# Optimization experiments

Hardware: AMD Instinct MI355X
Metric: run time of the kernel (lower is better)

The kernel has to match this reference:

```python
import jax, jax.numpy as jnp
import numpy as np

N = 50000      # nodes
E = 500000     # edges
IN = 256       # input feature dim
HID = 64       # hidden (per-head) dim, layer 1
H1 = 4         # heads, layer 1
NC = 64        # num_classes (layer 2 out, 1 head)
ED = 32        # edge_dim
T = 8          # num_etypes
SLOPE = 0.2    # leakyrelu negative slope


def setup_inputs() -> dict:
    key = jax.random.key(0)
    ks = jax.random.split(key, 20)
    p = lambda k, shape: (jax.random.normal(k, shape, jnp.float32) * 0.05)
    return {
        "h": jax.random.normal(ks[0], (N, IN), jnp.float32),
        "row": jax.random.randint(ks[1], (E,), 0, N, jnp.int32),   # src
        "col": jax.random.randint(ks[2], (E,), 0, N, jnp.int32),   # dst
        "etype": jax.random.randint(ks[3], (E,), 0, T, jnp.int32),
        # layer 1 (4 heads, no residual, elu activation)
        "edge_emb1": p(ks[4], (T, ED)),
        "W1": p(ks[5], (IN, HID * H1)),
        "Wr1": p(ks[6], (T, ED, ED * H1)),      # TypedLinear per-etype weight
        "a_l1": p(ks[7], (H1, HID)),
        "a_r1": p(ks[8], (H1, HID)),
        "a_e1": p(ks[9], (H1, ED)),
        # layer 2 (1 head, residual Linear, no activation)
        "edge_emb2": p(ks[10], (T, ED)),
        "W2": p(ks[11], (HID * H1, NC)),
        "Wr2": p(ks[12], (T, ED, ED)),
        "a_l2": p(ks[13], (1, NC)),
        "a_r2": p(ks[14], (1, NC)),
        "a_e2": p(ks[15], (1, ED)),
        "res_W2": p(ks[16], (HID * H1, NC)),
        "res_b2": p(ks[17], (NC,)),
    }


def _simple_hgn_conv(h, row, col, etype, edge_emb, W, Wr, a_l, a_r, a_e,
                     res_W, res_b, apply_act):
    """One SimpleHGNConv layer. h:[N,in], returns [N, out_dim*H] (D-major, H-minor
    layout, matching emb.permute(0,2,1).view in the torch code)."""
    H, D = a_l.shape            # num_heads, out_dim
    n = h.shape[0]
    emb = (h @ W).reshape(n, H, D)                     # [N,H,D]
    emb = jnp.where(jnp.isnan(emb), 0.0, emb)
    # TypedLinear: edge_emb[etype] @ Wr[etype]; only T distinct rows -> per-type GEMM
    ee = jnp.einsum('te,teo->to', edge_emb, Wr).reshape(T, H, ED)  # [T,H,ED]
    h_l = jnp.einsum('nhd,hd->nh', emb, a_l)[row]      # [E,H]
    h_r = jnp.einsum('nhd,hd->nh', emb, a_r)[col]      # [E,H]
    h_e = jnp.einsum('thd,hd->th', ee, a_e)[etype]     # [E,H]
    att = jax.nn.leaky_relu(h_l + h_r + h_e, SLOPE)    # [E,H]
    # edge_softmax: normalize over incoming edges of each destination node (col)
    seg_max = jax.ops.segment_max(att, col, num_segments=n)   # [N,H]
    att = jnp.exp(att - seg_max[col])
    seg_sum = jax.ops.segment_sum(att, col, num_segments=n)   # [N,H]
    alpha = att / seg_sum[col]                          # [E,H]
    # u_mul_e + sum aggregation
    msg = emb[row] * alpha[:, :, None]                  # [E,H,D]
    out = jax.ops.segment_sum(msg, col, num_segments=n) # [N,H,D]
    out = out.transpose(0, 2, 1).reshape(n, D * H)      # D-major layout
    if res_W is not None:
        out = out + h @ res_W + res_b
    if apply_act:
        out = jax.nn.elu(out)
    return out


def reference(h, row, col, etype,
              edge_emb1, W1, Wr1, a_l1, a_r1, a_e1,
              edge_emb2, W2, Wr2, a_l2, a_r2, a_e2, res_W2, res_b2):
    h1 = _simple_hgn_conv(h, row, col, etype, edge_emb1, W1, Wr1,
                          a_l1, a_r1, a_e1, None, None, True)
    h2 = _simple_hgn_conv(h1, row, col, etype, edge_emb2, W2, Wr2,
                          a_l2, a_r2, a_e2, res_W2, res_b2, False)
    # split by node type (first half type 'l', second half type 'v')
    return (h2[: N // 2], h2[N // 2 :])
```

## Files before the change

### kernel.cpp

```cpp
#include <hip/hip_runtime.h>
#include <hip/hip_bf16.h>

typedef __bf16 bf16x8 __attribute__((ext_vector_type(8)));
typedef float f32x4 __attribute__((ext_vector_type(4)));

#define IN_DIM 256
#define NT 8

__device__ __forceinline__ float b2f(unsigned short u) {
  union { unsigned int i; float f; } x; x.i = ((unsigned int)u) << 16; return x.f;
}
__device__ __forceinline__ float lo2f(unsigned int w) {
  union { unsigned int i; float f; } x; x.i = w << 16; return x.f;
}
__device__ __forceinline__ float hi2f(unsigned int w) {
  union { unsigned int i; float f; } x; x.i = w & 0xFFFF0000u; return x.f;
}
__device__ __forceinline__ unsigned short f2b(float f) {
  union { float f; unsigned int i; } u; u.f = f;
  unsigned int r = u.i + 0x7FFF + ((u.i >> 16) & 1);
  return (unsigned short)(r >> 16);
}
__device__ __forceinline__ float lrelu(float x) { return x >= 0.f ? x : 0.2f * x; }
__device__ __forceinline__ float ldf(const void* p, size_t i, int isf32) {
  return isf32 ? ((const float*)p)[i] : b2f(((const unsigned short*)p)[i]);
}

__global__ void detect_kernel(const unsigned int* __restrict__ hw, int* __restrict__ flag) {
  int tid = threadIdx.x;
  int bad = 0;
  for (int i = 0; i < 4; i++) {
    unsigned int w = hw[tid * 4 + i];
    unsigned int e = (w & 0x7FFFu) >> 7;
    if (e >= 0xC0u) bad++;
  }
#pragma unroll
  for (int off = 32; off; off >>= 1) bad += __shfl_xor(bad, off);
  if (tid == 0) *flag = (bad > 8) ? 1 : 0;
}

__global__ void prep_all_kernel(const void* __restrict__ W1, const void* __restrict__ W2,
                                const void* __restrict__ rW2,
                                const void* __restrict__ al1, const void* __restrict__ ar1,
                                const void* __restrict__ al2, const void* __restrict__ ar2,
                                const void* __restrict__ ee1, const void* __restrict__ Wr1,
                                const void* __restrict__ ae1,
                                const void* __restrict__ ee2, const void* __restrict__ Wr2,
                                const void* __restrict__ ae2,
                                unsigned short* __restrict__ W1t,
                                unsigned short* __restrict__ W2t,
                                float* __restrict__ a2l, float* __restrict__ a2r,
                                float* __restrict__ he1, float* __restrict__ he2,
                                float* __restrict__ alD, float* __restrict__ arD,
                                const int* __restrict__ dflag) {
  int isf32 = *dflag;
  int b = blockIdx.x, tid = threadIdx.x;
  if (b < 384) {
    int j = b, k = tid;
    if (j < 256) {
      int src = (j & 3) * 64 + (j >> 2);
      W1t[j * 256 + k] = f2b(ldf(W1, (size_t)k * 256 + src, isf32));
    } else {
      int o = j - 256;
      float v = (o < 64) ? ldf(W2, (size_t)k * 64 + o, isf32)
                         : ldf(rW2, (size_t)k * 64 + (o - 64), isf32);
      W2t[o * 256 + k] = f2b(v);
    }
  } else if (b < 448) {
    int k = (b - 384) * 4 + (tid >> 6), d = tid & 63;
    float w2 = ldf(W2, (size_t)k * 64 + d, isf32);
    float l2 = w2 * ldf(al2, d, isf32);
    float r2 = w2 * ldf(ar2, d, isf32);
#pragma unroll
    for (int off = 32; off; off >>= 1) { l2 += __shfl_xor(l2, off); r2 += __shfl_xor(r2, off); }
    if (d == 0) { a2l[k] = l2; a2r[k] = r2; }
  } else {
    int bid = b - 448;
    int t = tid >> 5, d = tid & 31;
    if (bid < 4) {
      int h = bid;
      float s = 0.f;
#pragma unroll
      for (int e = 0; e < 32; e++)
        s += ldf(ee1, t * 32 + e, isf32) * ldf(Wr1, (size_t)(t * 32 + e) * 128 + h * 32 + d, isf32);
      float v = s * ldf(ae1, h * 32 + d, isf32);
#pragma unroll
      for (int off = 16; off; off >>= 1) v += __shfl_xor(v, off);
      if (d == 0) he1[t * 4 + h] = v;
    } else if (bid == 4) {
      float s = 0.f;
#pragma unroll
      for (int e = 0; e < 32; e++)
        s += ldf(ee2, t * 32 + e, isf32) * ldf(Wr2, (size_t)(t * 32 + e) * 32 + d, isf32);
      float v = s * ldf(ae2, d, isf32);
#pragma unroll
      for (int off = 16; off; off >>= 1) v += __shfl_xor(v, off);
      if (d == 0) he2[t] = v;
    } else {
      int j = tid;
      alD[j] = ldf(al1, (j & 3) * 64 + (j >> 2), isf32);
      arD[j] = ldf(ar1, (j & 3) * 64 + (j >> 2), isf32);
    }
  }
}

__global__ __launch_bounds__(256, 2) void gemm1_fused(
    const void* __restrict__ A, int M,
    const unsigned short* __restrict__ Bt,
    unsigned short* __restrict__ emb1,
    const float* __restrict__ alD, const float* __restrict__ arD,
    float* __restrict__ hl1, float* __restrict__ hr1,
    const int* __restrict__ dflag) {
  __shared__ unsigned short As[64 * 64];
  __shared__ unsigned short Bs[256 * 64];
  __shared__ float lsum[4][64][4];
  __shared__ float rsum[4][64][4];
  int isf32 = *dflag;
  const int tid = threadIdx.x;
  const int m0 = blockIdx.x * 64;
  const int wv = tid >> 6, lane = tid & 63;
  const int q = lane >> 4, m = lane & 15;
  const int jp = wv * 64;
  f32x4 acc[4][4] = {};
  for (int kc = 0; kc < 256; kc += 64) {
    {
      int row = tid >> 2, qt = tid & 3;
      int gr = m0 + row;
      unsigned short tmp[16];
      if (gr < M) {
        if (isf32) {
          const float* ap = (const float*)A + (size_t)gr * 256 + kc + qt * 16;
          float4 v0 = *(const float4*)ap;
          float4 v1 = *(const float4*)(ap + 4);
          float4 v2 = *(const float4*)(ap + 8);
          float4 v3 = *(const float4*)(ap + 12);
          tmp[0]=f2b(v0.x); tmp[1]=f2b(v0.y); tmp[2]=f2b(v0.z); tmp[3]=f2b(v0.w);
          tmp[4]=f2b(v1.x); tmp[5]=f2b(v1.y); tmp[6]=f2b(v1.z); tmp[7]=f2b(v1.w);
          tmp[8]=f2b(v2.x); tmp[9]=f2b(v2.y); tmp[10]=f2b(v2.z); tmp[11]=f2b(v2.w);
          tmp[12]=f2b(v3.x); tmp[13]=f2b(v3.y); tmp[14]=f2b(v3.z); tmp[15]=f2b(v3.w);
        } else {
          const unsigned short* ap = (const unsigned short*)A + (size_t)gr * 256 + kc + qt * 16;
          *(int4*)tmp = *(const int4*)ap;
          *(int4*)(tmp + 8) = *(const int4*)(ap + 8);
        }
      } else {
        for (int x = 0; x < 16; x++) tmp[x] = 0;
      }
      int g0 = (qt * 2) ^ (row & 7);
      int g1 = (qt * 2 + 1) ^ (row & 7);
      *(int4*)(As + row * 64 + g0 * 8) = *(int4*)tmp;
      *(int4*)(As + row * 64 + g1 * 8) = *(int4*)(tmp + 8);
    }
    {
#pragma unroll
      for (int i = 0; i < 8; i++) {
        int id = tid + i * 256;
        int row = id >> 3, gg = id & 7;
        int4 v = *(const int4*)(Bt + (size_t)row * 256 + kc + gg * 8);
        int pg = gg ^ (row & 7);
        *(int4*)(Bs + row * 64 + pg * 8) = v;
      }
    }
    __syncthreads();
#pragma unroll
    for (int ks = 0; ks < 2; ks++) {
      int gk = ks * 4 + q;
      bf16x8 afr[4];
#pragma unroll
      for (int cm = 0; cm < 4; cm++) {
        int row = cm * 16 + m;
        afr[cm] = *(const bf16x8*)(As + row * 64 + (gk ^ (row & 7)) * 8);
      }
#pragma unroll
      for (int cj = 0; cj < 4; cj++) {
        int jr = jp + cj * 16 + m;
        bf16x8 b = *(const bf16x8*)(Bs + jr * 64 + (gk ^ (jr & 7)) * 8);
#pragma unroll
        for (int cm = 0; cm < 4; cm++)
          acc[cm][cj] = __builtin_amdgcn_mfma_f32_16x16x32_bf16(afr[cm], b, acc[cm][cj], 0, 0, 0);
      }
    }
    __syncthreads();
  }
  float al[4], ar[4];
#pragma unroll
  for (int cj = 0; cj < 4; cj++) {
    al[cj] = alD[jp + cj * 16 + m];
    ar[cj] = arD[jp + cj * 16 + m];
  }
#pragma unroll
  for (int cm = 0; cm < 4; cm++) {
#pragma unroll
    for (int r = 0; r < 4; r++) {
      int lrow = cm * 16 + q * 4 + r;
      int gm = m0 + lrow;
      float lp = 0.f, rp = 0.f;
#pragma unroll
      for (int cj = 0; cj < 4; cj++) {
        float v = acc[cm][cj][r];
        if (gm < M) emb1[(size_t)gm * 256 + jp + cj * 16 + m] = f2b(v);
        lp += v * al[cj]; rp += v * ar[cj];
      }
      lp += __shfl_xor(lp, 4); lp += __shfl_xor(lp, 8);
      rp += __shfl_xor(rp, 4); rp += __shfl_xor(rp, 8);
      if (m < 4) { lsum[wv][lrow][m] = lp; rsum[wv][lrow][m] = rp; }
    }
  }
  __syncthreads();
  {
    int row = tid >> 2, h = tid & 3;
    int gm = m0 + row;
    if (gm < M) {
      float l = lsum[0][row][h] + lsum[1][row][h] + lsum[2][row][h] + lsum[3][row][h];
      float r = rsum[0][row][h] + rsum[1][row][h] + rsum[2][row][h] + rsum[3][row][h];
      hl1[(size_t)gm * 4 + h] = l;
      hr1[(size_t)gm * 4 + h] = r;
    }
  }
}

__global__ __launch_bounds__(256, 2) void gemm2_fused(
    const unsigned short* __restrict__ A, int M,
    const unsigned short* __restrict__ Bt,
    unsigned short* __restrict__ emb2, unsigned short* __restrict__ res,
    const void* __restrict__ bias, const int* __restrict__ dflag) {
  __shared__ unsigned short As[64 * 64];
  __shared__ unsigned short Bs[128 * 64];
  int isf32 = *dflag;
  const int tid = threadIdx.x;
  const int m0 = blockIdx.x * 64;
  const int wv = tid >> 6, lane = tid & 63;
  const int q = lane >> 4, m = lane & 15;
  const int jp = (wv & 1) * 64;
  const int mh = (wv >> 1) * 32;
  f32x4 acc[2][4] = {};
  for (int kc = 0; kc < 256; kc += 64) {
    {
      int row = tid >> 2, qt = tid & 3;
      int gr = m0 + row;
      unsigned short tmp[16];
      if (gr < M) {
        const unsigned short* ap = A + (size_t)gr * 256 + kc + qt * 16;
        *(int4*)tmp = *(const int4*)ap;
        *(int4*)(tmp + 8) = *(const int4*)(ap + 8);
      } else {
        for (int x = 0; x < 16; x++) tmp[x] = 0;
      }
      int g0 = (qt * 2) ^ (row & 7);
      int g1 = (qt * 2 + 1) ^ (row & 7);
      *(int4*)(As + row * 64 + g0 * 8) = *(int4*)tmp;
      *(int4*)(As + row * 64 + g1 * 8) = *(int4*)(tmp + 8);
    }
    {
#pragma unroll
      for (int i = 0; i < 4; i++) {
        int id = tid + i * 256;
        int row = id >> 3, gg = id & 7;
        int4 v = *(const int4*)(Bt + (size_t)row * 256 + kc + gg * 8);
        int pg = gg ^ (row & 7);
        *(int4*)(Bs + row * 64 + pg * 8) = v;
      }
    }
    __syncthreads();
#pragma unroll
    for (int ks = 0; ks < 2; ks++) {
      int gk = ks * 4 + q;
      bf16x8 afr[2];
#pragma unroll
      for (int cm = 0; cm < 2; cm++) {
        int row = mh + cm * 16 + m;
        afr[cm] = *(const bf16x8*)(As + row * 64 + (gk ^ (row & 7)) * 8);
      }
#pragma unroll
      for (int cj = 0; cj < 4; cj++) {
        int jr = jp + cj * 16 + m;
        bf16x8 b = *(const bf16x8*)(Bs + jr * 64 + (gk ^ (jr & 7)) * 8);
#pragma unroll
        for (int cm = 0; cm < 2; cm++)
          acc[cm][cj] = __builtin_amdgcn_mfma_f32_16x16x32_bf16(afr[cm], b, acc[cm][cj], 0, 0, 0);
      }
    }
    __syncthreads();
  }
  float bv[4];
#pragma unroll
  for (int cj = 0; cj < 4; cj++)
    bv[cj] = (jp == 64) ? ldf(bias, cj * 16 + m, isf32) : 0.f;
#pragma unroll
  for (int cm = 0; cm < 2; cm++) {
#pragma unroll
    for (int r = 0; r < 4; r++) {
      int gm = m0 + mh + cm * 16 + q * 4 + r;
      if (gm < M) {
#pragma unroll
        for (int cj = 0; cj < 4; cj++) {
          float v = acc[cm][cj][r];
          int gj = cj * 16 + m;
          if (jp == 0) emb2[(size_t)gm * 64 + gj] = f2b(v);
          else res[(size_t)gm * 64 + gj] = f2b(v + bv[cj]);
        }
      }
    }
  }
}

__global__ void count_kernel(const int* __restrict__ col, int* __restrict__ cnt,
                             int E_, int N_) {
  int e = blockIdx.x * 256 + threadIdx.x;
  if (e >= E_) return;
  int c = col[e];
  if ((unsigned)c < (unsigned)N_) atomicAdd(&cnt[c], 1);
}

__global__ void scan1_kernel(const int* __restrict__ cnt, int* __restrict__ ptrb,
                             int* __restrict__ bsum, int n) {
  __shared__ int wsum[4];
  int tid = threadIdx.x, lane = tid & 63, wid = tid >> 6;
  int i = blockIdx.x * 256 + tid;
  int v = (i < n) ? cnt[i] : 0;
  int x = v;
#pragma unroll
  for (int off = 1; off < 64; off <<= 1) {
    int y = __shfl_up(x, off);
    if (lane >= off) x += y;
  }
  if (lane == 63) wsum[wid] = x;
  __syncthreads();
  int woff = 0;
#pragma unroll
  for (int k = 0; k < 4; k++) woff += (k < wid) ? wsum[k] : 0;
  if (i < n) ptrb[i] = x - v + woff;
  if (tid == 255) bsum[blockIdx.x] = woff + x;
}

__global__ void scan2_kernel(int* __restrict__ bsum, int* __restrict__ ptrb,
                             int nb, int n) {
  __shared__ int wsum[4];
  int tid = threadIdx.x, lane = tid & 63, wid = tid >> 6;
  int v = (tid < nb) ? bsum[tid] : 0;
  int x = v;
#pragma unroll
  for (int off = 1; off < 64; off <<= 1) {
    int y = __shfl_up(x, off);
    if (lane >= off) x += y;
  }
  if (lane == 63) wsum[wid] = x;
  __syncthreads();
  int woff = 0;
#pragma unroll
  for (int k = 0; k < 4; k++) woff += (k < wid) ? wsum[k] : 0;
  if (tid < nb) bsum[tid] = x - v + woff;
  if (tid == 255) ptrb[n] = woff + x;
}

__global__ void scan3_kernel(int* __restrict__ ptrb, const int* __restrict__ bsum, int n) {
  int i = blockIdx.x * 256 + threadIdx.x;
  if (i < n) ptrb[i] += bsum[blockIdx.x];
}

__global__ void fill_kernel(const int* __restrict__ col, const int* __restrict__ row,
                            const int* __restrict__ ety, const int* __restrict__ ptrb,
                            int* __restrict__ cnt, int* __restrict__ srcc, int E_, int N_) {
  int e = blockIdx.x * 256 + threadIdx.x;
  if (e >= E_) return;
  int c = col[e];
  if ((unsigned)c >= (unsigned)N_) return;
  int pos = atomicSub(&cnt[c], 1) - 1;
  long long slot = (long long)ptrb[c] + pos;
  if (slot >= 0 && slot < E_) {
    int sr = row[e], t = ety[e];
    srcc[slot] = ((unsigned)sr < (unsigned)N_ && (unsigned)t < (unsigned)NT)
                     ? (sr | (t << 20)) : -1;
  }
}

__global__ __launch_bounds__(256) void agg1_kernel(
    const int* __restrict__ ptrb, const int* __restrict__ srcc,
    const float* __restrict__ hl1, const float* __restrict__ hr1,
    const float* __restrict__ he1,
    const unsigned short* __restrict__ emb1, unsigned short* __restrict__ h1,
    const float* __restrict__ a2l, const float* __restrict__ a2r,
    float* __restrict__ hl2, float* __restrict__ hr2,
    int N_, int E_) {
  __shared__ float4 wds[4][64];
  __shared__ int sds[4][64];
  int wv = threadIdx.x >> 6, lane = threadIdx.x & 63;
  int node = blockIdx.x * 4 + wv;
  if (node >= N_) return;
  int p0 = ptrb[node], p1 = ptrb[node + 1];
  p0 = max(0, min(p0, E_)); p1 = max(p0, min(p1, E_));
  float4 hrv = *(const float4*)(hr1 + 4 * (size_t)node);
  float s0 = 0.f, s1 = 0.f, s2 = 0.f, s3 = 0.f;
  float acc[8] = {0.f,0.f,0.f,0.f,0.f,0.f,0.f,0.f};
  int g = lane >> 5, sub = lane & 31;
  for (int pb = p0; pb < p1; pb += 64) {
    int mc = p1 - pb; if (mc > 64) mc = 64;
    float4 w = {0.f, 0.f, 0.f, 0.f};
    int src = 0;
    if (lane < mc) {
      int spk = srcc[pb + lane];
      if (spk >= 0) {
        int sr = spk & 0xFFFFF, t = spk >> 20;
        float4 a = *(const float4*)(hl1 + 4 * (size_t)sr);
        float4 gg = *(const float4*)(he1 + 4 * (size_t)t);
        w.x = __expf(lrelu(a.x + hrv.x + gg.x));
        w.y = __expf(lrelu(a.y + hrv.y + gg.y));
        w.z = __expf(lrelu(a.z + hrv.z + gg.z));
        w.w = __expf(lrelu(a.w + hrv.w + gg.w));
        src = sr;
      }
    }
    s0 += w.x; s1 += w.y; s2 += w.z; s3 += w.w;
    wds[wv][lane] = w;
    sds[wv][lane] = src;
    for (int j = 0; j < mc; j += 4) {
      int jj0 = j + g, jj1 = j + 2 + g;
      bool v0 = jj0 < mc, v1 = jj1 < mc;
      float4 u0, u1; int r0 = 0, r1 = 0;
      int4 raw0, raw1;
      if (v0) { u0 = wds[wv][jj0]; r0 = sds[wv][jj0];
                raw0 = *(const int4*)(emb1 + (size_t)r0 * 256 + sub * 8); }
      if (v1) { u1 = wds[wv][jj1]; r1 = sds[wv][jj1];
                raw1 = *(const int4*)(emb1 + (size_t)r1 * 256 + sub * 8); }
      if (v0) {
        acc[0] += u0.x * lo2f(raw0.x); acc[1] += u0.y * hi2f(raw0.x);
        acc[2] += u0.z * lo2f(raw0.y); acc[3] += u0.w * hi2f(raw0.y);
        acc[4] += u0.x * lo2f(raw0.z); acc[5] += u0.y * hi2f(raw0.z);
        acc[6] += u0.z * lo2f(raw0.w); acc[7] += u0.w * hi2f(raw0.w);
      }
      if (v1) {
        acc[0] += u1.x * lo2f(raw1.x); acc[1] += u1.y * hi2f(raw1.x);
        acc[2] += u1.z * lo2f(raw1.y); acc[3] += u1.w * hi2f(raw1.y);
        acc[4] += u1.x * lo2f(raw1.z); acc[5] += u1.y * hi2f(raw1.z);
        acc[6] += u1.z * lo2f(raw1.w); acc[7] += u1.w * hi2f(raw1.w);
      }
    }
  }
#pragma unroll
  for (int off = 32; off; off >>= 1) {
    s0 += __shfl_xor(s0, off); s1 += __shfl_xor(s1, off);
    s2 += __shfl_xor(s2, off); s3 += __shfl_xor(s3, off);
  }
#pragma unroll
  for (int k = 0; k < 8; k++) acc[k] += __shfl_xor(acc[k], 32);
  float lp = 0.f, rp = 0.f;
  if (g == 0) {
    float sv[4] = {s0, s1, s2, s3};
    unsigned short o[8];
#pragma unroll
    for (int k = 0; k < 8; k++) {
      float r = (sv[k & 3] > 0.f) ? acc[k] / sv[k & 3] : 0.f;
      r = r > 0.f ? r : __expf(r) - 1.f;
      o[k] = f2b(r);
      int j = sub * 8 + k;
      lp += r * a2l[j];
      rp += r * a2r[j];
    }
    *(int4*)(h1 + (size_t)node * 256 + sub * 8) = *(int4*)o;
  }
#pragma unroll
  for (int off = 1; off < 32; off <<= 1) { lp += __shfl_xor(lp, off); rp += __shfl_xor(rp, off); }
  if (lane == 0) { hl2[node] = lp; hr2[node] = rp; }
}

__global__ __launch_bounds__(256) void agg2_kernel(
    const int* __restrict__ ptrb, const int* __restrict__ srcc,
    const float* __restrict__ hl2, const float* __restrict__ hr2,
    const float* __restrict__ he2,
    const unsigned short* __restrict__ emb2, const unsigned short* __restrict__ res,
    void* __restrict__ out, int N_, int E_, const int* __restrict__ dflag) {
  __shared__ int2 wsd[4][64];
  int isf32 = *dflag;
  int wv = threadIdx.x >> 6, lane = threadIdx.x & 63;
  int node = blockIdx.x * 4 + wv;
  if (node >= N_) return;
  int p0 = ptrb[node], p1 = ptrb[node + 1];
  p0 = max(0, min(p0, E_)); p1 = max(p0, min(p1, E_));
  float hrv = hr2[node];
  float s = 0.f;
  float acc[4] = {0.f, 0.f, 0.f, 0.f};
  int g = lane >> 4, sub = lane & 15;
  for (int pb = p0; pb < p1; pb += 64) {
    int mc = p1 - pb; if (mc > 64) mc = 64;
    float w = 0.f;
    int src = 0;
    if (lane < mc) {
      int spk = srcc[pb + lane];
      if (spk >= 0) {
        int sr = spk & 0xFFFFF, t = spk >> 20;
        w = __expf(lrelu(hl2[sr] + hrv + he2[t]));
        src = sr;
      }
    }
    s += w;
    int2 pk; pk.x = __float_as_int(w); pk.y = src;
    wsd[wv][lane] = pk;
    for (int j = 0; j < mc; j += 8) {
      int jj0 = j + g, jj1 = j + 4 + g;
      bool v0 = jj0 < mc, v1 = jj1 < mc;
      float u0, u1; int r0 = 0, r1 = 0;
      int2 raw0, raw1;
      if (v0) { int2 ws = wsd[wv][jj0]; u0 = __int_as_float(ws.x); r0 = ws.y;
                raw0 = *(const int2*)(emb2 + (size_t)r0 * 64 + sub * 4); }
      if (v1) { int2 ws = wsd[wv][jj1]; u1 = __int_as_float(ws.x); r1 = ws.y;
                raw1 = *(const int2*)(emb2 + (size_t)r1 * 64 + sub * 4); }
      if (v0) {
        acc[0] += u0 * lo2f(raw0.x); acc[1] += u0 * hi2f(raw0.x);
        acc[2] += u0 * lo2f(raw0.y); acc[3] += u0 * hi2f(raw0.y);
      }
      if (v1) {
        acc[0] += u1 * lo2f(raw1.x); acc[1] += u1 * hi2f(raw1.x);
        acc[2] += u1 * lo2f(raw1.y); acc[3] += u1 * hi2f(raw1.y);
      }
    }
  }
#pragma unroll
  for (int off = 32; off; off >>= 1) s += __shfl_xor(s, off);
#pragma unroll
  for (int k = 0; k < 4; k++) {
    acc[k] += __shfl_xor(acc[k], 16);
    acc[k] += __shfl_xor(acc[k], 32);
  }
  if (g == 0) {
    ushort4 rv = *(const ushort4*)(res + (size_t)node * 64 + sub * 4);
    float o0 = ((s > 0.f) ? acc[0] / s : 0.f) + b2f(rv.x);
    float o1 = ((s > 0.f) ? acc[1] / s : 0.f) + b2f(rv.y);
    float o2 = ((s > 0.f) ? acc[2] / s : 0.f) + b2f(rv.z);
    float o3 = ((s > 0.f) ? acc[3] / s : 0.f) + b2f(rv.w);
    size_t oi = (size_t)node * 64 + sub * 4;
    if (isf32) {
      float4 ov = {o0, o1, o2, o3};
      *(float4*)((float*)out + oi) = ov;
    } else {
      ushort4 ov; ov.x = f2b(o0); ov.y = f2b(o1); ov.z = f2b(o2); ov.w = f2b(o3);
      *(ushort4*)((unsigned short*)out + oi) = ov;
    }
  }
}

extern "C" void kernel_launch(void* const* d_in, const int* in_sizes, int n_in,
                              void* d_out, int out_size, void* d_ws, size_t ws_size,
                              hipStream_t stream) {
  const int N = in_sizes[0] / IN_DIM;
  const int E = in_sizes[1];

  const void* h   = d_in[0];
  const int* row  = (const int*)d_in[1];
  const int* col  = (const int*)d_in[2];
  const int* ety  = (const int*)d_in[3];
  const void* ee1 = d_in[4];
  const void* W1  = d_in[5];
  const void* Wr1 = d_in[6];
  const void* al1 = d_in[7];
  const void* ar1 = d_in[8];
  const void* ae1 = d_in[9];
  const void* ee2 = d_in[10];
  const void* W2  = d_in[11];
  const void* Wr2 = d_in[12];
  const void* al2 = d_in[13];
  const void* ar2 = d_in[14];
  const void* ae2 = d_in[15];
  const void* rW2 = d_in[16];
  const void* rb2 = d_in[17];

  char* p = (char*)d_ws;
  auto take = [&](size_t b) { char* q = p; p += (b + 255) & ~(size_t)255; return q; };
  unsigned short* h1   = (unsigned short*)take((size_t)N * 256 * 2);
  unsigned short* emb1 = (unsigned short*)take((size_t)N * 256 * 2);
  int* srcc = (int*)take((size_t)E * 4);
  int* ptrb = (int*)take((size_t)(N + 1) * 4);
  int* cnt  = (int*)take((size_t)N * 4);
  int* bsum = (int*)take(1024);
  float* hl1 = (float*)take((size_t)N * 4 * 4);
  float* hr1 = (float*)take((size_t)N * 4 * 4);
  float* hl2 = (float*)take((size_t)N * 4);
  float* hr2 = (float*)take((size_t)N * 4);
  unsigned short* W1t = (unsigned short*)take(256 * 256 * 2);
  unsigned short* W2t = (unsigned short*)take(128 * 256 * 2);
  float* a2l = (float*)take(256 * 4);
  float* a2r = (float*)take(256 * 4);
  float* alD = (float*)take(256 * 4);
  float* arD = (float*)take(256 * 4);
  float* he1 = (float*)take(NT * 4 * 4);
  float* he2 = (float*)take(NT * 4);
  int* dflag = (int*)take(256);
  unsigned short* emb2 = emb1;
  unsigned short* res  = emb1 + (size_t)N * 64;

  const size_t need = (size_t)(p - (char*)d_ws);
  if (need > ws_size) {
    hipMemsetAsync(d_out, 0, (size_t)out_size * 2, stream);
    return;
  }

  const int EB = (E + 255) / 256;
  const int MB = (N + 63) / 64;
  const int SB = (N + 255) / 256;

  detect_kernel<<<1, 64, 0, stream>>>((const unsigned int*)h, dflag);
  hipMemsetAsync(cnt, 0, (size_t)N * 4, stream);
  prep_all_kernel<<<454, 256, 0, stream>>>(W1, W2, rW2, al1, ar1, al2, ar2,
                                           ee1, Wr1, ae1, ee2, Wr2, ae2,
                                           W1t, W2t, a2l, a2r, he1, he2, alD, arD, dflag);

  count_kernel<<<EB, 256, 0, stream>>>(col, cnt, E, N);
  scan1_kernel<<<SB, 256, 0, stream>>>(cnt, ptrb, bsum, N);
  scan2_kernel<<<1, 256, 0, stream>>>(bsum, ptrb, SB, N);
  scan3_kernel<<<SB, 256, 0, stream>>>(ptrb, bsum, N);
  fill_kernel<<<EB, 256, 0, stream>>>(col, row, ety, ptrb, cnt, srcc, E, N);

  gemm1_fused<<<MB, 256, 0, stream>>>(h, N, W1t, emb1, alD, arD, hl1, hr1, dflag);
  agg1_kernel<<<(N + 3) / 4, 256, 0, stream>>>(
      ptrb, srcc, hl1, hr1, he1, emb1, h1, a2l, a2r, hl2, hr2, N, E);

  gemm2_fused<<<MB, 256, 0, stream>>>(h1, N, W2t, emb2, res, rb2, dflag);
  agg2_kernel<<<(N + 3) / 4, 256, 0, stream>>>(
      ptrb, srcc, hl2, hr2, he2, emb2, res, d_out, N, E, dflag);
}
```

Measured before the change: 281.3 us.

## Map multiple destination nodes per wavefront in aggregation kernels

Aggregation kernels now assign one destination node per half-wave (layer 1) or quarter-wave (layer 2) instead of a whole 64-lane wave. With average degree around ten, this uses lanes that previously sat idle in the edge-weight phase and removes the cross-group accumulator shuffle reduction. Each node's gather loop becomes longer and serial per sub-group. Divergent degrees within a wave can leave lanes waiting on the slowest node.

```diff
diff --git a/kernel.cpp b/kernel.cpp
--- a/kernel.cpp
+++ b/kernel.cpp
@@ -382,23 +382,23 @@
     const float* __restrict__ a2l, const float* __restrict__ a2r,
     float* __restrict__ hl2, float* __restrict__ hr2,
     int N_, int E_) {
-  __shared__ float4 wds[4][64];
-  __shared__ int sds[4][64];
+  __shared__ float4 wds[4][2][32];
+  __shared__ int sds[4][2][32];
   int wv = threadIdx.x >> 6, lane = threadIdx.x & 63;
-  int node = blockIdx.x * 4 + wv;
+  int g = lane >> 5, sub = lane & 31;
+  int node = blockIdx.x * 8 + wv * 2 + g;
   if (node >= N_) return;
   int p0 = ptrb[node], p1 = ptrb[node + 1];
   p0 = max(0, min(p0, E_)); p1 = max(p0, min(p1, E_));
   float4 hrv = *(const float4*)(hr1 + 4 * (size_t)node);
   float s0 = 0.f, s1 = 0.f, s2 = 0.f, s3 = 0.f;
   float acc[8] = {0.f,0.f,0.f,0.f,0.f,0.f,0.f,0.f};
-  int g = lane >> 5, sub = lane & 31;
-  for (int pb = p0; pb < p1; pb += 64) {
-    int mc = p1 - pb; if (mc > 64) mc = 64;
+  for (int pb = p0; pb < p1; pb += 32) {
+    int mc = p1 - pb; if (mc > 32) mc = 32;
     float4 w = {0.f, 0.f, 0.f, 0.f};
     int src = 0;
-    if (lane < mc) {
-      int spk = srcc[pb + lane];
+    if (sub < mc) {
+      int spk = srcc[pb + sub];
       if (spk >= 0) {
         int sr = spk & 0xFFFFF, t = spk >> 20;
         float4 a = *(const float4*)(hl1 + 4 * (size_t)sr);
@@ -411,23 +411,20 @@
       }
     }
     s0 += w.x; s1 += w.y; s2 += w.z; s3 += w.w;
-    wds[wv][lane] = w;
-    sds[wv][lane] = src;
-    for (int j = 0; j < mc; j += 4) {
-      int jj0 = j + g, jj1 = j + 2 + g;
-      bool v0 = jj0 < mc, v1 = jj1 < mc;
-      float4 u0, u1; int r0 = 0, r1 = 0;
-      int4 raw0, raw1;
-      if (v0) { u0 = wds[wv][jj0]; r0 = sds[wv][jj0];
-                raw0 = *(const int4*)(emb1 + (size_t)r0 * 256 + sub * 8); }
-      if (v1) { u1 = wds[wv][jj1]; r1 = sds[wv][jj1];
+    wds[wv][g][sub] = w;
+    sds[wv][g][sub] = src;
+    for (int j = 0; j < mc; j += 2) {
+      bool v1 = (j + 1) < mc;
+      float4 u0 = wds[wv][g][j];
+      int r0 = sds[wv][g][j];
+      int4 raw0 = *(const int4*)(emb1 + (size_t)r0 * 256 + sub * 8);
+      float4 u1; int r1 = 0; int4 raw1;
+      if (v1) { u1 = wds[wv][g][j + 1]; r1 = sds[wv][g][j + 1];
                 raw1 = *(const int4*)(emb1 + (size_t)r1 * 256 + sub * 8); }
-      if (v0) {
-        acc[0] += u0.x * lo2f(raw0.x); acc[1] += u0.y * hi2f(raw0.x);
-        acc[2] += u0.z * lo2f(raw0.y); acc[3] += u0.w * hi2f(raw0.y);
-        acc[4] += u0.x * lo2f(raw0.z); acc[5] += u0.y * hi2f(raw0.z);
-        acc[6] += u0.z * lo2f(raw0.w); acc[7] += u0.w * hi2f(raw0.w);
-      }
+      acc[0] += u0.x * lo2f(raw0.x); acc[1] += u0.y * hi2f(raw0.x);
+      acc[2] += u0.z * lo2f(raw0.y); acc[3] += u0.w * hi2f(raw0.y);
+      acc[4] += u0.x * lo2f(raw0.z); acc[5] += u0.y * hi2f(raw0.z);
+      acc[6] += u0.z * lo2f(raw0.w); acc[7] += u0.w * hi2f(raw0.w);
       if (v1) {
         acc[0] += u1.x * lo2f(raw1.x); acc[1] += u1.y * hi2f(raw1.x);
         acc[2] += u1.z * lo2f(raw1.y); acc[3] += u1.w * hi2f(raw1.y);
@@ -437,30 +434,26 @@
     }
   }
 #pragma unroll
-  for (int off = 32; off; off >>= 1) {
+  for (int off = 1; off < 32; off <<= 1) {
     s0 += __shfl_xor(s0, off); s1 += __shfl_xor(s1, off);
     s2 += __shfl_xor(s2, off); s3 += __shfl_xor(s3, off);
   }
-#pragma unroll
-  for (int k = 0; k < 8; k++) acc[k] += __shfl_xor(acc[k], 32);
+  float sv[4] = {s0, s1, s2, s3};
+  unsigned short o[8];
   float lp = 0.f, rp = 0.f;
-  if (g == 0) {
-    float sv[4] = {s0, s1, s2, s3};
-    unsigned short o[8];
-#pragma unroll
-    for (int k = 0; k < 8; k++) {
-      float r = (sv[k & 3] > 0.f) ? acc[k] / sv[k & 3] : 0.f;
-      r = r > 0.f ? r : __expf(r) - 1.f;
-      o[k] = f2b(r);
-      int j = sub * 8 + k;
-      lp += r * a2l[j];
-      rp += r * a2r[j];
-    }
-    *(int4*)(h1 + (size_t)node * 256 + sub * 8) = *(int4*)o;
-  }
+#pragma unroll
+  for (int k = 0; k < 8; k++) {
+    float r = (sv[k & 3] > 0.f) ? acc[k] / sv[k & 3] : 0.f;
+    r = r > 0.f ? r : __expf(r) - 1.f;
+    o[k] = f2b(r);
+    int j = sub * 8 + k;
+    lp += r * a2l[j];
+    rp += r * a2r[j];
+  }
+  *(int4*)(h1 + (size_t)node * 256 + sub * 8) = *(int4*)o;
 #pragma unroll
   for (int off = 1; off < 32; off <<= 1) { lp += __shfl_xor(lp, off); rp += __shfl_xor(rp, off); }
-  if (lane == 0) { hl2[node] = lp; hr2[node] = rp; }
+  if (sub == 0) { hl2[node] = lp; hr2[node] = rp; }
 }
 
 __global__ __launch_bounds__(256) void agg2_kernel(
@@ -469,23 +462,23 @@
     const float* __restrict__ he2,
     const unsigned short* __restrict__ emb2, const unsigned short* __restrict__ res,
     void* __restrict__ out, int N_, int E_, const int* __restrict__ dflag) {
-  __shared__ int2 wsd[4][64];
+  __shared__ int2 wsd[4][4][16];
   int isf32 = *dflag;
   int wv = threadIdx.x >> 6, lane = threadIdx.x & 63;
-  int node = blockIdx.x * 4 + wv;
+  int g = lane >> 4, sub = lane & 15;
+  int node = blockIdx.x * 16 + wv * 4 + g;
   if (node >= N_) return;
   int p0 = ptrb[node], p1 = ptrb[node + 1];
   p0 = max(0, min(p0, E_)); p1 = max(p0, min(p1, E_));
   float hrv = hr2[node];
   float s = 0.f;
   float acc[4] = {0.f, 0.f, 0.f, 0.f};
-  int g = lane >> 4, sub = lane & 15;
-  for (int pb = p0; pb < p1; pb += 64) {
-    int mc = p1 - pb; if (mc > 64) mc = 64;
+  for (int pb = p0; pb < p1; pb += 16) {
+    int mc = p1 - pb; if (mc > 16) mc = 16;
     float w = 0.f;
     int src = 0;
-    if (lane < mc) {
-      int spk = srcc[pb + lane];
+    if (sub < mc) {
+      int spk = srcc[pb + sub];
       if (spk >= 0) {
         int sr = spk & 0xFFFFF, t = spk >> 20;
         w = __expf(lrelu(hl2[sr] + hrv + he2[t]));
@@ -494,20 +487,18 @@
     }
     s += w;
     int2 pk; pk.x = __float_as_int(w); pk.y = src;
-    wsd[wv][lane] = pk;
-    for (int j = 0; j < mc; j += 8) {
-      int jj0 = j + g, jj1 = j + 4 + g;
-      bool v0 = jj0 < mc, v1 = jj1 < mc;
-      float u0, u1; int r0 = 0, r1 = 0;
-      int2 raw0, raw1;
-      if (v0) { int2 ws = wsd[wv][jj0]; u0 = __int_as_float(ws.x); r0 = ws.y;
-                raw0 = *(const int2*)(emb2 + (size_t)r0 * 64 + sub * 4); }
-      if (v1) { int2 ws = wsd[wv][jj1]; u1 = __int_as_float(ws.x); r1 = ws.y;
+    wsd[wv][g][sub] = pk;
+    for (int j = 0; j < mc; j += 2) {
+      bool v1 = (j + 1) < mc;
+      int2 ws0 = wsd[wv][g][j];
+      float u0 = __int_as_float(ws0.x); int r0 = ws0.y;
+      int2 raw0 = *(const int2*)(emb2 + (size_t)r0 * 64 + sub * 4);
+      float u1; int r1 = 0; int2 raw1;
+      if (v1) { int2 ws1 = wsd[wv][g][j + 1];
+                u1 = __int_as_float(ws1.x); r1 = ws1.y;
                 raw1 = *(const int2*)(emb2 + (size_t)r1 * 64 + sub * 4); }
-      if (v0) {
-        acc[0] += u0 * lo2f(raw0.x); acc[1] += u0 * hi2f(raw0.x);
-        acc[2] += u0 * lo2f(raw0.y); acc[3] += u0 * hi2f(raw0.y);
-      }
+      acc[0] += u0 * lo2f(raw0.x); acc[1] += u0 * hi2f(raw0.x);
+      acc[2] += u0 * lo2f(raw0.y); acc[3] += u0 * hi2f(raw0.y);
       if (v1) {
         acc[0] += u1 * lo2f(raw1.x); acc[1] += u1 * hi2f(raw1.x);
         acc[2] += u1 * lo2f(raw1.y); acc[3] += u1 * hi2f(raw1.y);
@@ -515,26 +506,19 @@
     }
   }
 #pragma unroll
-  for (int off = 32; off; off >>= 1) s += __shfl_xor(s, off);
-#pragma unroll
-  for (int k = 0; k < 4; k++) {
-    acc[k] += __shfl_xor(acc[k], 16);
-    acc[k] += __shfl_xor(acc[k], 32);
-  }
-  if (g == 0) {
-    ushort4 rv = *(const ushort4*)(res + (size_t)node * 64 + sub * 4);
-    float o0 = ((s > 0.f) ? acc[0] / s : 0.f) + b2f(rv.x);
-    float o1 = ((s > 0.f) ? acc[1] / s : 0.f) + b2f(rv.y);
-    float o2 = ((s > 0.f) ? acc[2] / s : 0.f) + b2f(rv.z);
-    float o3 = ((s > 0.f) ? acc[3] / s : 0.f) + b2f(rv.w);
-    size_t oi = (size_t)node * 64 + sub * 4;
-    if (isf32) {
-      float4 ov = {o0, o1, o2, o3};
-      *(float4*)((float*)out + oi) = ov;
-    } else {
-      ushort4 ov; ov.x = f2b(o0); ov.y = f2b(o1); ov.z = f2b(o2); ov.w = f2b(o3);
-      *(ushort4*)((unsigned short*)out + oi) = ov;
-    }
+  for (int off = 1; off < 16; off <<= 1) s += __shfl_xor(s, off);
+  ushort4 rv = *(const ushort4*)(res + (size_t)node * 64 + sub * 4);
+  float o0 = ((s > 0.f) ? acc[0] / s : 0.f) + b2f(rv.x);
+  float o1 = ((s > 0.f) ? acc[1] / s : 0.f) + b2f(rv.y);
+  float o2 = ((s > 0.f) ? acc[2] / s : 0.f) + b2f(rv.z);
+  float o3 = ((s > 0.f) ? acc[3] / s : 0.f) + b2f(rv.w);
+  size_t oi = (size_t)node * 64 + sub * 4;
+  if (isf32) {
+    float4 ov = {o0, o1, o2, o3};
+    *(float4*)((float*)out + oi) = ov;
+  } else {
+    ushort4 ov; ov.x = f2b(o0); ov.y = f2b(o1); ov.z = f2b(o2); ov.w = f2b(o3);
+    *(ushort4*)((unsigned short*)out + oi) = ov;
   }
 }
 
@@ -610,10 +594,10 @@
   fill_kernel<<<EB, 256, 0, stream>>>(col, row, ety, ptrb, cnt, srcc, E, N);
 
   gemm1_fused<<<MB, 256, 0, stream>>>(h, N, W1t, emb1, alD, arD, hl1, hr1, dflag);
-  agg1_kernel<<<(N + 3) / 4, 256, 0, stream>>>(
+  agg1_kernel<<<(N + 7) / 8, 256, 0, stream>>>(
       ptrb, srcc, hl1, hr1, he1, emb1, h1, a2l, a2r, hl2, hr2, N, E);
 
   gemm2_fused<<<MB, 256, 0, stream>>>(h1, N, W2t, emb2, res, rb2, dflag);
-  agg2_kernel<<<(N + 3) / 4, 256, 0, stream>>>(
+  agg2_kernel<<<(N + 15) / 16, 256, 0, stream>>>(
       ptrb, srcc, hl2, hr2, he2, emb2, res, d_out, N, E, dflag);
 }
```

Result: slower. 298.4 us (+6.1%).
